# Optimization experiments

Hardware: AMD Instinct MI355X
Metric: run time of the kernel (lower is better)

Reference implementation:

```python
import jax, jax.numpy as jnp
import numpy as np

N_LAYERS = 6
D_MODEL = 272          # num_variables
D_STATE = 64           # d_state
D_INNER = 2 * D_MODEL  # expand=2 -> 544
D_CONV = 4
DT_RANK = 17           # ceil(272/16)
N_SCORES = 4
B, L = 4, 2048


def setup_inputs():
    key = jax.random.key(0)
    ks = jax.random.split(key, 10)
    def rn(k, shape, s=0.02):
        return jax.random.normal(k, shape, dtype=jnp.float32) * s
    A_init = jnp.broadcast_to(jnp.arange(1, D_STATE + 1, dtype=jnp.float32), (N_LAYERS, D_INNER, D_STATE))
    return {
        "x": jax.random.normal(ks[0], (B, L, D_MODEL), dtype=jnp.float32),
        "ln_w": jnp.ones((N_LAYERS, D_MODEL), jnp.float32),
        "ln_b": jnp.zeros((N_LAYERS, D_MODEL), jnp.float32),
        "in_proj_w": rn(ks[1], (N_LAYERS, 2 * D_INNER, D_MODEL)),
        "conv_w": rn(ks[2], (N_LAYERS, D_INNER, D_CONV), 0.2),
        "conv_b": jnp.zeros((N_LAYERS, D_INNER), jnp.float32),
        "x_proj_w": rn(ks[3], (N_LAYERS, DT_RANK + 2 * D_STATE, D_INNER)),
        "dt_proj_w": rn(ks[4], (N_LAYERS, D_INNER, DT_RANK), 0.1),
        "dt_proj_b": rn(ks[5], (N_LAYERS, D_INNER), 0.5),
        "A_log": jnp.log(A_init),
        "Dskip": jnp.ones((N_LAYERS, D_INNER), jnp.float32),
        "out_proj_w": rn(ks[6], (N_LAYERS, D_MODEL, D_INNER)),
        "reg_w": rn(ks[7], (N_SCORES, D_MODEL)),
        "reg_b": jnp.zeros((N_SCORES,), jnp.float32),
    }


def _layernorm(x, w, b, eps=1e-5):
    mu = x.mean(-1, keepdims=True)
    var = ((x - mu) ** 2).mean(-1, keepdims=True)
    return (x - mu) * jax.lax.rsqrt(var + eps) * w + b


def _selective_scan(u, delta, A, Bm, C, Dd):
    # u, delta: (b,l,d); Bm, C: (b,l,n); A: (d,n); Dd: (d,)
    def step(h, inp):
        d_t, B_t, C_t, u_t = inp                           # (b,d),(b,n),(b,n),(b,d)
        dA = jnp.exp(d_t[:, :, None] * A)                  # (b,d,n)
        h = dA * h + (d_t * u_t)[:, :, None] * B_t[:, None, :]
        return h, jnp.einsum('bdn,bn->bd', h, C_t)
    h0 = jnp.zeros((u.shape[0], A.shape[0], A.shape[1]), u.dtype)
    xs = tuple(jnp.swapaxes(a, 0, 1) for a in (delta, Bm, C, u))  # time-major
    _, ys = jax.lax.scan(step, h0, xs)
    return jnp.swapaxes(ys, 0, 1) + u * Dd


def _mamba_block(x, ln_w, ln_b, Wi, cw, cb, Wx, Wdt, bdt, A_log, Dd, Wo):
    h = _layernorm(x, ln_w, ln_b)
    xi, z = jnp.split(h @ Wi.T, 2, axis=-1)                # (b,l,d_inner) each
    xp = jnp.pad(xi, ((0, 0), (D_CONV - 1, 0), (0, 0)))    # causal depthwise conv
    xc = sum(xp[:, k:k + xi.shape[1], :] * cw[:, k] for k in range(D_CONV)) + cb
    xc = jax.nn.silu(xc)
    dbl = xc @ Wx.T                                        # (b,l,dt_rank+2n)
    dt, Bm, C = jnp.split(dbl, [DT_RANK, DT_RANK + D_STATE], axis=-1)
    delta = jax.nn.softplus(dt @ Wdt.T + bdt)
    y = _selective_scan(xc, delta, -jnp.exp(A_log), Bm, C, Dd)
    y = y * jax.nn.silu(z)
    return x + y @ Wo.T                                    # residual


def reference(x, ln_w, ln_b, in_proj_w, conv_w, conv_b, x_proj_w, dt_proj_w, dt_proj_b, A_log, Dskip, out_proj_w, reg_w, reg_b):
    for i in range(N_LAYERS):
        x = _mamba_block(x, ln_w[i], ln_b[i], in_proj_w[i], conv_w[i], conv_b[i],
                         x_proj_w[i], dt_proj_w[i], dt_proj_b[i], A_log[i], Dskip[i], out_proj_w[i])
    feat = x.mean(axis=1)                                  # (b, d_model)
    scores = feat @ reg_w.T + reg_b                        # (b, n_scores)
    return (scores, feat)
```

## Files before the change

kernel.cpp:

```cpp
#include <hip/hip_runtime.h>
#include <hip/hip_bf16.h>
#include <math.h>

#define NL 6
#define DM 272
#define DS 64
#define DI 544
#define DTR 17
#define NSC 4
#define BB 4
#define LL 2048
#define MTOK (BB*LL)
#define TCH 128
#define CH  16
#define DQ  (DI/4)

typedef __attribute__((ext_vector_type(8))) short bf16x8;
typedef __attribute__((ext_vector_type(4))) float f32x4;

__device__ __forceinline__ float sigmoidf_(float x){ return 1.0f/(1.0f+__expf(-x)); }
__device__ __forceinline__ unsigned short f2bfu(float x){
    union { __hip_bfloat16 h; unsigned short u; } c; c.h = __float2bfloat16(x); return c.u;
}
__device__ __forceinline__ float bfu2f(unsigned short u){ return __uint_as_float(((unsigned)u)<<16); }
__device__ __forceinline__ float exp2x(float x){ float r; asm("v_exp_f32 %0, %1" : "=v"(r) : "v"(x)); return r; }
__device__ __forceinline__ float log2x(float x){ float r; asm("v_log_f32 %0, %1" : "=v"(r) : "v"(x)); return r; }
__device__ __forceinline__ float softplus_(float s){
    float sp = 0.6931471806f * log2x(1.0f + exp2x(s * 1.44269504f));
    return (s > 20.f) ? s : sp;
}

#define DPPADD(x, ctrl) x += __int_as_float(__builtin_amdgcn_update_dpp(0, __float_as_int(x), ctrl, 0xf, 0xf, true))
__device__ __forceinline__ float wsum64(float x){
    DPPADD(x, 0x111); DPPADD(x, 0x112); DPPADD(x, 0x114); DPPADD(x, 0x118);
    DPPADD(x, 0x142); DPPADD(x, 0x143);
    return x;
}

__global__ __launch_bounds__(256) void ln_kernel(const float* __restrict__ X,
                          const float* __restrict__ w,
                          const float* __restrict__ b,
                          unsigned short* __restrict__ Hb)
{
    int wave = threadIdx.x >> 6;
    int lane = threadIdx.x & 63;
    int tok = blockIdx.x*4 + wave;
    const float* xr = X + (size_t)tok*DM;
    float v[5];
    float s=0.f, ss=0.f;
    #pragma unroll
    for (int j=0;j<5;++j){
        int idx = lane + j*64;
        float x = (idx < DM) ? xr[idx] : 0.f;
        v[j]=x; s+=x; ss+=x*x;
    }
    #pragma unroll
    for (int off=1; off<64; off<<=1){ s += __shfl_xor(s,off); ss += __shfl_xor(ss,off); }
    float mu  = s * (1.0f/DM);
    float var = ss*(1.0f/DM) - mu*mu;
    float inv = 1.0f/sqrtf(var + 1e-5f);
    unsigned short* hr = Hb + (size_t)tok*DM;
    #pragma unroll
    for (int j=0;j<5;++j){
        int idx = lane + j*64;
        if (idx<DM) hr[idx] = f2bfu((v[j]-mu)*inv*w[idx] + b[idx]);
    }
}

template<bool RESID, bool OUTBF16>
__global__ __launch_bounds__(256) void gmfma(const unsigned short* __restrict__ A, int lda,
                     const unsigned short* __restrict__ W, int ldw,
                     void* __restrict__ Cv, int ldc,
                     const float* __restrict__ R, int ldr,
                     int N, int K)
{
    __shared__ unsigned short As[128*40];
    __shared__ unsigned short Bs[128*40];
    int bm = blockIdx.x*128, bn = blockIdx.y*128;
    int tid = threadIdx.x;
    int lane = tid & 63, wave = tid >> 6;
    int wm = wave >> 1, wn = wave & 1;
    f32x4 acc[4][4] = {};
    int r16 = lane & 15, kg = (lane >> 4) * 8;
    for (int k0=0; k0<K; k0+=32){
        #pragma unroll
        for (int it=0; it<2; ++it){
            int cid = tid + it*256;
            int row = cid >> 2, kq = (cid & 3)*8;
            int kk = k0 + kq;
            uint4 za = make_uint4(0,0,0,0);
            if (kk < K) za = *(const uint4*)(A + (size_t)(bm+row)*lda + kk);
            *(uint4*)&As[row*40 + kq] = za;
            uint4 zb = make_uint4(0,0,0,0);
            int wr = bn + row;
            if (wr < N && kk < K) zb = *(const uint4*)(W + (size_t)wr*ldw + kk);
            *(uint4*)&Bs[row*40 + kq] = zb;
        }
        __syncthreads();
        bf16x8 af[4], bfr[4];
        #pragma unroll
        for (int mi=0; mi<4; ++mi)
            af[mi] = *(bf16x8*)&As[(wm*64 + mi*16 + r16)*40 + kg];
        #pragma unroll
        for (int ni=0; ni<4; ++ni)
            bfr[ni] = *(bf16x8*)&Bs[(wn*64 + ni*16 + r16)*40 + kg];
        #pragma unroll
        for (int mi=0; mi<4; ++mi)
            #pragma unroll
            for (int ni=0; ni<4; ++ni)
                acc[mi][ni] = __builtin_amdgcn_mfma_f32_16x16x32_bf16(af[mi], bfr[ni], acc[mi][ni], 0, 0, 0);
        __syncthreads();
    }
    int rowt = (lane >> 4)*4, colt = lane & 15;
    #pragma unroll
    for (int mi=0; mi<4; ++mi){
        #pragma unroll
        for (int ni=0; ni<4; ++ni){
            int col = bn + wn*64 + ni*16 + colt;
            if (col < N){
                #pragma unroll
                for (int j=0; j<4; ++j){
                    int row = bm + wm*64 + mi*16 + rowt + j;
                    float v = acc[mi][ni][j];
                    if (RESID) v += R[(size_t)row*ldr + col];
                    if (OUTBF16)
                        ((unsigned short*)Cv)[(size_t)row*ldc + col] = f2bfu(v);
                    else
                        ((float*)Cv)[(size_t)row*ldc + col] = v;
                }
            }
        }
    }
}

__global__ __launch_bounds__(256) void conv_t2_kernel(const unsigned short* __restrict__ XZb,
                                 const float* __restrict__ cw,
                                 const float* __restrict__ cb,
                                 unsigned int* __restrict__ UGt,
                                 unsigned short* __restrict__ XCb)
{
    __shared__ float xi[67][69];
    __shared__ float zz[64][69];
    int bid = blockIdx.x;
    int b  = bid >> 8;
    int rem = bid & 255;
    int t0 = (rem >> 3)*64;
    int d0 = (rem & 7)*68;
    int tid = threadIdx.x;
    for (int li = tid; li < 67*17; li += 256){
        int row = li / 17, q = li - row*17;
        int tg = t0 - 3 + row;
        float4 v = make_float4(0.f,0.f,0.f,0.f);
        if (tg >= 0){
            ushort4 u4 = *(const ushort4*)(XZb + ((size_t)b*LL + tg)*(2*DI) + d0 + q*4);
            v.x = bfu2f(u4.x); v.y = bfu2f(u4.y); v.z = bfu2f(u4.z); v.w = bfu2f(u4.w);
        }
        xi[row][q*4+0]=v.x; xi[row][q*4+1]=v.y; xi[row][q*4+2]=v.z; xi[row][q*4+3]=v.w;
    }
    for (int li = tid; li < 64*17; li += 256){
        int row = li / 17, q = li - row*17;
        ushort4 u4 = *(const ushort4*)(XZb + ((size_t)b*LL + t0 + row)*(2*DI) + DI + d0 + q*4);
        zz[row][q*4+0]=bfu2f(u4.x); zz[row][q*4+1]=bfu2f(u4.y);
        zz[row][q*4+2]=bfu2f(u4.z); zz[row][q*4+3]=bfu2f(u4.w);
    }
    __syncthreads();
    int t = tid & 63;
    int dw = tid >> 6;
    float xcreg[17];
    #pragma unroll
    for (int i=0; i<17; ++i){
        int dl = dw + i*4;
        int d = d0 + dl;
        const float* cwd = cw + d*4;
        float acc = cb[d];
        #pragma unroll
        for (int k=0;k<4;++k) acc = fmaf(xi[t+k][dl], cwd[k], acc);
        float xc = acc * sigmoidf_(acc);
        float z  = zz[t][dl];
        size_t o = ((size_t)b*DI + d)*LL + t0 + t;
        float g = z * sigmoidf_(z);
        UGt[o] = (unsigned int)f2bfu(xc) | ((unsigned int)f2bfu(g) << 16);
        xcreg[i] = xc;
    }
    __syncthreads();
    #pragma unroll
    for (int i=0; i<17; ++i) zz[t][dw + i*4] = xcreg[i];
    __syncthreads();
    for (int li = tid; li < 64*17; li += 256){
        int row = li / 17, q = li - row*17;
        ushort4 v;
        v.x = f2bfu(zz[row][q*4+0]); v.y = f2bfu(zz[row][q*4+1]);
        v.z = f2bfu(zz[row][q*4+2]); v.w = f2bfu(zz[row][q*4+3]);
        *(ushort4*)&XCb[((size_t)b*LL + t0 + row)*DI + d0 + q*4] = v;
    }
}

__global__ __launch_bounds__(256) void scan_a(const unsigned int* __restrict__ UGt,
                       const float* __restrict__ DBLb,
                       const float* __restrict__ Wdt,
                       const float* __restrict__ bdt,
                       const float* __restrict__ A_log,
                       float* __restrict__ Q,
                       float* __restrict__ S,
                       unsigned short* __restrict__ DELtb)
{
    __shared__ float2 dlb[4][4][64];
    int tid = threadIdx.x;
    int wave = tid >> 6, lane = tid & 63;
    float2 (*Db)[64] = dlb[wave];
    int wid = blockIdx.x*4 + wave;
    int dd = wid % DQ;
    int c  = (wid / DQ) % CH;
    int b  = wid / (DQ*CH);
    int d0 = dd, d1 = dd+DQ, d2 = dd+2*DQ, d3 = dd+3*DQ;
    const float L2E = 1.44269504f;
    float Av0 = -__expf(A_log[d0*DS + lane]) * L2E;
    float Av1 = -__expf(A_log[d1*DS + lane]) * L2E;
    float Av2 = -__expf(A_log[d2*DS + lane]) * L2E;
    float Av3 = -__expf(A_log[d3*DS + lane]) * L2E;
    const float* wd0 = Wdt + d0*DTR;
    const float* wd1 = Wdt + d1*DTR;
    const float* wd2 = Wdt + d2*DTR;
    const float* wd3 = Wdt + d3*DTR;
    float h0=0.f,h1=0.f,h2=0.f,h3=0.f, ds0=0.f,ds1=0.f,ds2=0.f,ds3=0.f;
    size_t rb0 = ((size_t)b*DI + d0)*LL + c*TCH;
    size_t rb1 = ((size_t)b*DI + d1)*LL + c*TCH;
    size_t rb2 = ((size_t)b*DI + d2)*LL + c*TCH;
    size_t rb3 = ((size_t)b*DI + d3)*LL + c*TCH;
    const float* pB = DBLb + ((size_t)b*LL + (size_t)c*TCH)*145;
    for (int blk=0; blk<TCH/64; ++blk){
        const float* dp = pB + (size_t)(blk*64 + lane)*145;
        float s0=bdt[d0], s1=bdt[d1], s2=bdt[d2], s3=bdt[d3];
        #pragma unroll
        for (int r=0;r<17;++r){
            float d = dp[r];
            s0 = fmaf(d, wd0[r], s0);
            s1 = fmaf(d, wd1[r], s1);
            s2 = fmaf(d, wd2[r], s2);
            s3 = fmaf(d, wd3[r], s3);
        }
        float dl0 = softplus_(s0), dl1 = softplus_(s1);
        float dl2 = softplus_(s2), dl3 = softplus_(s3);
        size_t o0 = rb0 + blk*64 + lane, o1 = rb1 + blk*64 + lane;
        size_t o2 = rb2 + blk*64 + lane, o3 = rb3 + blk*64 + lane;
        DELtb[o0] = f2bfu(dl0); DELtb[o1] = f2bfu(dl1);
        DELtb[o2] = f2bfu(dl2); DELtb[o3] = f2bfu(dl3);
        float du0 = dl0*bfu2f((unsigned short)UGt[o0]);
        float du1 = dl1*bfu2f((unsigned short)UGt[o1]);
        float du2 = dl2*bfu2f((unsigned short)UGt[o2]);
        float du3 = dl3*bfu2f((unsigned short)UGt[o3]);
        ds0 += dl0; ds1 += dl1; ds2 += dl2; ds3 += dl3;
        Db[0][lane] = make_float2(dl0, du0);
        Db[1][lane] = make_float2(dl1, du1);
        Db[2][lane] = make_float2(dl2, du2);
        Db[3][lane] = make_float2(dl3, du3);
        const float* p = pB + (size_t)blk*64*145;
        #pragma unroll 1
        for (int g=0; g<8; ++g){
            const float2* q0 = &Db[0][g*8];
            const float2* q1 = &Db[1][g*8];
            const float2* q2 = &Db[2][g*8];
            const float2* q3 = &Db[3][g*8];
            #pragma unroll
            for (int i=0; i<8; ++i){
                float Bv = p[17+lane];
                float2 a0=q0[i], a1=q1[i], a2=q2[i], a3=q3[i];
                h0 = fmaf(exp2x(a0.x*Av0), h0, a0.y*Bv);
                h1 = fmaf(exp2x(a1.x*Av1), h1, a1.y*Bv);
                h2 = fmaf(exp2x(a2.x*Av2), h2, a2.y*Bv);
                h3 = fmaf(exp2x(a3.x*Av3), h3, a3.y*Bv);
                p += 145;
            }
        }
    }
    size_t q0i = ((size_t)b*DI + d0)*CH + c, q1i = ((size_t)b*DI + d1)*CH + c;
    size_t q2i = ((size_t)b*DI + d2)*CH + c, q3i = ((size_t)b*DI + d3)*CH + c;
    Q[q0i*64 + lane] = h0; Q[q1i*64 + lane] = h1;
    Q[q2i*64 + lane] = h2; Q[q3i*64 + lane] = h3;
    float s0w = wsum64(ds0), s1w = wsum64(ds1), s2w = wsum64(ds2), s3w = wsum64(ds3);
    if (lane == 63){ S[q0i]=s0w; S[q1i]=s1w; S[q2i]=s2w; S[q3i]=s3w; }
}

__global__ __launch_bounds__(256) void scan_c(const unsigned int* __restrict__ UGt,
                       const unsigned short* __restrict__ DELtb,
                       const float* __restrict__ DBLb,
                       const float* __restrict__ A_log,
                       const float* __restrict__ Dskip,
                       const float* __restrict__ Q,
                       const float* __restrict__ S,
                       unsigned short* __restrict__ Yb)
{
    __shared__ float P[4][2][4][76];
    __shared__ float Ypark[4][2][4];
    __shared__ float2 dlb[4][2][64];
    __shared__ unsigned short Yst[64][12];
    int tid = threadIdx.x;
    int wave = tid >> 6, lane = tid & 63;
    float (*Pr0)[76] = P[wave][0];
    float (*Pr1)[76] = P[wave][1];
    float* Yp0 = Ypark[wave][0];
    float* Yp1 = Ypark[wave][1];
    float2* Db0 = dlb[wave][0];
    float2* Db1 = dlb[wave][1];
    int wid = blockIdx.x*4 + wave;
    int dd = wid % (DI/2);
    int c  = (wid / (DI/2)) % CH;
    int b  = wid / ((DI/2)*CH);
    int d0 = dd, d1 = dd + DI/2;
    int wid0 = blockIdx.x*4;
    int dd0b = wid0 % (DI/2);
    int cB = (wid0 / (DI/2)) % CH;
    int bB = wid0 / ((DI/2)*CH);
    const float L2E = 1.44269504f;
    float Av0 = -__expf(A_log[d0*DS + lane]) * L2E;
    float Av1 = -__expf(A_log[d1*DS + lane]) * L2E;
    float Dd0 = Dskip[d0], Dd1 = Dskip[d1];
    size_t q0 = ((size_t)b*DI + d0)*CH, q1 = ((size_t)b*DI + d1)*CH;
    float h0=0.f, h1=0.f;
    for (int j=0; j<c; ++j){
        h0 = fmaf(exp2x(Av0*S[q0+j]), h0, Q[(q0+j)*64 + lane]);
        h1 = fmaf(exp2x(Av1*S[q1+j]), h1, Q[(q1+j)*64 + lane]);
    }
    size_t rb0 = ((size_t)b*DI + d0)*LL + c*TCH;
    size_t rb1 = ((size_t)b*DI + d1)*LL + c*TCH;
    const float* pB = DBLb + ((size_t)b*LL + c*TCH)*145;
    int fr = lane >> 4, fq = (lane & 15)*4;
    for (int blk=0; blk<TCH/64; ++blk){
        size_t o0 = rb0 + blk*64 + lane, o1 = rb1 + blk*64 + lane;
        float dl0 = bfu2f(DELtb[o0]), dl1 = bfu2f(DELtb[o1]);
        unsigned int ug0 = UGt[o0], ug1 = UGt[o1];
        float ul0 = bfu2f((unsigned short)ug0), ul1 = bfu2f((unsigned short)ug1);
        float gl0 = bfu2f((unsigned short)(ug0 >> 16)), gl1 = bfu2f((unsigned short)(ug1 >> 16));
        Db0[lane] = make_float2(dl0, dl0*ul0);
        Db1[lane] = make_float2(dl1, dl1*ul1);
        float y0=0.f, y1=0.f;
        const float* p = pB + (size_t)blk*64*145;
        #pragma unroll 1
        for (int f=0; f<16; ++f){
            const float2* db0 = &Db0[f*4];
            const float2* db1 = &Db1[f*4];
            #pragma unroll
            for (int i=0; i<4; ++i){
                float Bv = p[17+lane];
                float Cv = p[81+lane];
                float2 a0 = db0[i], a1 = db1[i];
                h0 = fmaf(exp2x(a0.x*Av0), h0, a0.y*Bv);
                h1 = fmaf(exp2x(a1.x*Av1), h1, a1.y*Bv);
                Pr0[i][lane] = h0*Cv;
                Pr1[i][lane] = h1*Cv;
                p += 145;
            }
            float4 xa0 = *(const float4*)&Pr0[fr][fq];
            float s0f = (xa0.x+xa0.y)+(xa0.z+xa0.w);
            DPPADD(s0f,0x111); DPPADD(s0f,0x112); DPPADD(s0f,0x114); DPPADD(s0f,0x118);
            float4 xa1 = *(const float4*)&Pr1[fr][fq];
            float s1f = (xa1.x+xa1.y)+(xa1.z+xa1.w);
            DPPADD(s1f,0x111); DPPADD(s1f,0x112); DPPADD(s1f,0x114); DPPADD(s1f,0x118);
            if ((lane & 15) == 15){ Yp0[fr] = s0f; Yp1[fr] = s1f; }
            float g0 = Yp0[lane & 3];
            float g1 = Yp1[lane & 3];
            if ((lane >> 2) == f){ y0 = g0; y1 = g1; }
        }
        Yst[lane][wave]     = f2bfu((y0 + ul0*Dd0)*gl0);
        Yst[lane][4 + wave] = f2bfu((y1 + ul1*Dd1)*gl1);
        __syncthreads();
        if (tid < 128){
            int row = tid & 63, grp = tid >> 6;
            ushort4 v = *(const ushort4*)&Yst[row][grp*4];
            size_t trow = (size_t)bB*LL + (size_t)cB*TCH + blk*64 + row;
            *(ushort4*)&Yb[trow*DI + dd0b + grp*(DI/2)] = v;
        }
        __syncthreads();
    }
}

__global__ __launch_bounds__(256) void wconv_kernel(const float* __restrict__ src,
                            unsigned short* __restrict__ dst,
                            int total, int kin, int kout)
{
    int idx = blockIdx.x*256 + threadIdx.x;
    if (idx >= total) return;
    int r = idx / kout, c = idx - r*kout;
    float v = (c < kin) ? src[(size_t)r*kin + c] : 0.f;
    dst[idx] = f2bfu(v);
}

__global__ __launch_bounds__(256) void head1_kernel(const float* __restrict__ X,
                             float* __restrict__ Pt)
{
    int b = blockIdx.x >> 6, c = blockIdx.x & 63;
    int tid = threadIdx.x;
    for (int dm = tid; dm < DM; dm += 256){
        float s = 0.f;
        const float* base = X + ((size_t)b*LL + c*32)*DM + dm;
        #pragma unroll 8
        for (int tt=0; tt<32; ++tt) s += base[(size_t)tt*DM];
        Pt[(size_t)(b*64 + c)*DM + dm] = s;
    }
}

__global__ __launch_bounds__(256) void head2_kernel(const float* __restrict__ Pt,
                             const float* __restrict__ reg_w,
                             const float* __restrict__ reg_b,
                             float* __restrict__ out)
{
    __shared__ float feat[DM];
    int b = blockIdx.x, tid = threadIdx.x;
    for (int dm = tid; dm < DM; dm += 256){
        float s = 0.f;
        for (int c=0; c<64; ++c) s += Pt[(size_t)(b*64 + c)*DM + dm];
        float f = s * (1.0f/LL);
        feat[dm] = f;
        out[16 + b*DM + dm] = f;
    }
    __syncthreads();
    if (tid < NSC){
        float s = reg_b[tid];
        const float* wr = reg_w + tid*DM;
        for (int k=0;k<DM;++k) s = fmaf(feat[k], wr[k], s);
        out[b*NSC + tid] = s;
    }
}

extern "C" void kernel_launch(void* const* d_in, const int* in_sizes, int n_in,
                              void* d_out, int out_size, void* d_ws, size_t ws_size,
                              hipStream_t stream)
{
    const float* x_in  = (const float*)d_in[0];
    const float* ln_w  = (const float*)d_in[1];
    const float* ln_b  = (const float*)d_in[2];
    const float* Wi    = (const float*)d_in[3];
    const float* cw    = (const float*)d_in[4];
    const float* cb    = (const float*)d_in[5];
    const float* Wx    = (const float*)d_in[6];
    const float* Wdt   = (const float*)d_in[7];
    const float* bdt   = (const float*)d_in[8];
    const float* A_log = (const float*)d_in[9];
    const float* Dd    = (const float*)d_in[10];
    const float* Wo    = (const float*)d_in[11];
    const float* regw  = (const float*)d_in[12];
    const float* regb  = (const float*)d_in[13];
    float* out = (float*)d_out;

    char* base = (char*)d_ws;
    auto carve = [&](size_t bytes) -> char* {
        char* p = base; base += (bytes + 255) & ~(size_t)255; return p;
    };
    unsigned short* XZb   = (unsigned short*)carve((size_t)MTOK*1088*2);
    unsigned int*   UGt   = (unsigned int*)carve((size_t)MTOK*544*4);
    unsigned short* DELtb = (unsigned short*)carve((size_t)MTOK*544*2);
    float*          DBLb  = (float*)carve((size_t)MTOK*145*4);
    float*          Xb    = (float*)carve((size_t)MTOK*272*4);
    unsigned short* Yb    = (unsigned short*)carve((size_t)MTOK*544*2);
    char*           SCR   = carve((size_t)MTOK*272*4);
    float*          Sbuf  = (float*)carve((size_t)BB*DI*CH*4);
    unsigned short* WiB   = (unsigned short*)carve((size_t)NL*1088*DM*2);
    unsigned short* WxB   = (unsigned short*)carve((size_t)NL*145*DI*2);
    unsigned short* WoB   = (unsigned short*)carve((size_t)NL*272*DI*2);

    unsigned short* Hb  = (unsigned short*)SCR;
    unsigned short* XCb = (unsigned short*)SCR;
    float*          Q   = (float*)SCR;
    float*          Pt  = (float*)SCR;

    (void)hipMemcpyAsync(Xb, x_in, sizeof(float)*(size_t)MTOK*DM, hipMemcpyDeviceToDevice, stream);

    wconv_kernel<<<(NL*1088*DM + 255)/256, 256, 0, stream>>>(Wi, WiB, NL*1088*DM, DM, DM);
    wconv_kernel<<<(NL*145*DI + 255)/256, 256, 0, stream>>>(Wx, WxB, NL*145*DI, DI, DI);
    wconv_kernel<<<(NL*272*DI + 255)/256, 256, 0, stream>>>(Wo, WoB, NL*272*DI, DI, DI);

    for (int l=0; l<NL; ++l){
        ln_kernel<<<MTOK/4, 256, 0, stream>>>(Xb, ln_w + l*DM, ln_b + l*DM, Hb);
        gmfma<false,true><<<dim3(MTOK/128, (2*DI+127)/128), 256, 0, stream>>>(
            Hb, DM, WiB + (size_t)l*2*DI*DM, DM, XZb, 2*DI, nullptr, 0, 2*DI, DM);
        conv_t2_kernel<<<BB*256, 256, 0, stream>>>(XZb, cw + l*DI*4, cb + l*DI, UGt, XCb);
        gmfma<false,false><<<dim3(MTOK/128, 2), 256, 0, stream>>>(
            XCb, DI, WxB + (size_t)l*145*DI, DI, DBLb, 145, nullptr, 0, 145, DI);
        scan_a<<<(BB*CH*DQ)/4, 256, 0, stream>>>(UGt, DBLb, Wdt + (size_t)l*DI*DTR, bdt + l*DI,
                                                 A_log + (size_t)l*DI*DS, Q, Sbuf, DELtb);
        scan_c<<<(BB*CH*(DI/2))/4, 256, 0, stream>>>(UGt, DELtb, DBLb,
                                                     A_log + (size_t)l*DI*DS, Dd + l*DI, Q, Sbuf, Yb);
        gmfma<true,false><<<dim3(MTOK/128, 3), 256, 0, stream>>>(
            Yb, DI, WoB + (size_t)l*DM*DI, DI, Xb, DM, Xb, DM, DM, DI);
    }
    head1_kernel<<<BB*64, 256, 0, stream>>>(Xb, Pt);
    head2_kernel<<<BB, 256, 0, stream>>>(Pt, regw, regb, out);
}
```

Baseline: 1.460 ms.

## Split x_proj output into dt buffer and packed bf16 B/C pairs for scans

The x_proj GEMM epilogue now writes the dt part to a compact fp32 buffer of 17 columns and packs B and C as interleaved bf16 pairs into one 32-bit word per state. The scan kernels read one packed word per lane per timestep instead of two separate fp32 loads at a 145-float stride, which cuts scan memory traffic and load count. scan_c also reads the delta/u pairs from shared memory as float4. The trade-off is lower precision for B and C, plus scattered 2-byte stores in the GEMM epilogue.

```diff
diff --git a/kernel.cpp b/kernel.cpp
--- a/kernel.cpp
+++ b/kernel.cpp
@@ -23,6 +23,8 @@
     union { __hip_bfloat16 h; unsigned short u; } c; c.h = __float2bfloat16(x); return c.u;
 }
 __device__ __forceinline__ float bfu2f(unsigned short u){ return __uint_as_float(((unsigned)u)<<16); }
+__device__ __forceinline__ float bclo(unsigned int bc){ return __uint_as_float(bc << 16); }
+__device__ __forceinline__ float bchi(unsigned int bc){ return __uint_as_float(bc & 0xffff0000u); }
 __device__ __forceinline__ float exp2x(float x){ float r; asm("v_exp_f32 %0, %1" : "=v"(r) : "v"(x)); return r; }
 __device__ __forceinline__ float log2x(float x){ float r; asm("v_log_f32 %0, %1" : "=v"(r) : "v"(x)); return r; }
 __device__ __forceinline__ float softplus_(float s){
@@ -67,11 +69,12 @@
     }
 }
 
-template<bool RESID, bool OUTBF16>
+template<int OMODE, bool RESID>
 __global__ __launch_bounds__(256) void gmfma(const unsigned short* __restrict__ A, int lda,
                      const unsigned short* __restrict__ W, int ldw,
                      void* __restrict__ Cv, int ldc,
                      const float* __restrict__ R, int ldr,
+                     void* __restrict__ aux,
                      int N, int K)
 {
     __shared__ unsigned short As[128*40];
@@ -123,10 +126,18 @@
                     int row = bm + wm*64 + mi*16 + rowt + j;
                     float v = acc[mi][ni][j];
                     if (RESID) v += R[(size_t)row*ldr + col];
-                    if (OUTBF16)
+                    if (OMODE == 0)
+                        ((float*)Cv)[(size_t)row*ldc + col] = v;
+                    else if (OMODE == 1)
                         ((unsigned short*)Cv)[(size_t)row*ldc + col] = f2bfu(v);
-                    else
-                        ((float*)Cv)[(size_t)row*ldc + col] = v;
+                    else {
+                        if (col < DTR)
+                            ((float*)Cv)[(size_t)row*DTR + col] = v;
+                        else if (col < DTR + DS)
+                            ((unsigned short*)aux)[((size_t)row*DS + col - DTR)*2] = f2bfu(v);
+                        else
+                            ((unsigned short*)aux)[((size_t)row*DS + col - DTR - DS)*2 + 1] = f2bfu(v);
+                    }
                 }
             }
         }
@@ -196,7 +207,8 @@
 }
 
 __global__ __launch_bounds__(256) void scan_a(const unsigned int* __restrict__ UGt,
-                       const float* __restrict__ DBLb,
+                       const float* __restrict__ DTb,
+                       const unsigned int* __restrict__ BCb,
                        const float* __restrict__ Wdt,
                        const float* __restrict__ bdt,
                        const float* __restrict__ A_log,
@@ -204,7 +216,7 @@
                        float* __restrict__ S,
                        unsigned short* __restrict__ DELtb)
 {
-    __shared__ float2 dlb[4][4][64];
+    __shared__ __align__(16) float2 dlb[4][4][64];
     int tid = threadIdx.x;
     int wave = tid >> 6, lane = tid & 63;
     float2 (*Db)[64] = dlb[wave];
@@ -223,13 +235,13 @@
     const float* wd2 = Wdt + d2*DTR;
     const float* wd3 = Wdt + d3*DTR;
     float h0=0.f,h1=0.f,h2=0.f,h3=0.f, ds0=0.f,ds1=0.f,ds2=0.f,ds3=0.f;
+    size_t tokBase = (size_t)b*LL + (size_t)c*TCH;
     size_t rb0 = ((size_t)b*DI + d0)*LL + c*TCH;
     size_t rb1 = ((size_t)b*DI + d1)*LL + c*TCH;
     size_t rb2 = ((size_t)b*DI + d2)*LL + c*TCH;
     size_t rb3 = ((size_t)b*DI + d3)*LL + c*TCH;
-    const float* pB = DBLb + ((size_t)b*LL + (size_t)c*TCH)*145;
     for (int blk=0; blk<TCH/64; ++blk){
-        const float* dp = pB + (size_t)(blk*64 + lane)*145;
+        const float* dp = DTb + (tokBase + blk*64 + lane)*DTR;
         float s0=bdt[d0], s1=bdt[d1], s2=bdt[d2], s3=bdt[d3];
         #pragma unroll
         for (int r=0;r<17;++r){
@@ -254,7 +266,7 @@
         Db[1][lane] = make_float2(dl1, du1);
         Db[2][lane] = make_float2(dl2, du2);
         Db[3][lane] = make_float2(dl3, du3);
-        const float* p = pB + (size_t)blk*64*145;
+        const unsigned int* pbc = BCb + (tokBase + blk*64)*DS;
         #pragma unroll 1
         for (int g=0; g<8; ++g){
             const float2* q0 = &Db[0][g*8];
@@ -263,13 +275,13 @@
             const float2* q3 = &Db[3][g*8];
             #pragma unroll
             for (int i=0; i<8; ++i){
-                float Bv = p[17+lane];
+                float Bv = bclo(pbc[lane]);
                 float2 a0=q0[i], a1=q1[i], a2=q2[i], a3=q3[i];
                 h0 = fmaf(exp2x(a0.x*Av0), h0, a0.y*Bv);
                 h1 = fmaf(exp2x(a1.x*Av1), h1, a1.y*Bv);
                 h2 = fmaf(exp2x(a2.x*Av2), h2, a2.y*Bv);
                 h3 = fmaf(exp2x(a3.x*Av3), h3, a3.y*Bv);
-                p += 145;
+                pbc += DS;
             }
         }
     }
@@ -283,7 +295,7 @@
 
 __global__ __launch_bounds__(256) void scan_c(const unsigned int* __restrict__ UGt,
                        const unsigned short* __restrict__ DELtb,
-                       const float* __restrict__ DBLb,
+                       const unsigned int* __restrict__ BCb,
                        const float* __restrict__ A_log,
                        const float* __restrict__ Dskip,
                        const float* __restrict__ Q,
@@ -292,7 +304,7 @@
 {
     __shared__ float P[4][2][4][76];
     __shared__ float Ypark[4][2][4];
-    __shared__ float2 dlb[4][2][64];
+    __shared__ __align__(16) float2 dlb[4][2][64];
     __shared__ unsigned short Yst[64][12];
     int tid = threadIdx.x;
     int wave = tid >> 6, lane = tid & 63;
@@ -321,9 +333,9 @@
         h0 = fmaf(exp2x(Av0*S[q0+j]), h0, Q[(q0+j)*64 + lane]);
         h1 = fmaf(exp2x(Av1*S[q1+j]), h1, Q[(q1+j)*64 + lane]);
     }
+    size_t tokBase = (size_t)b*LL + (size_t)c*TCH;
     size_t rb0 = ((size_t)b*DI + d0)*LL + c*TCH;
     size_t rb1 = ((size_t)b*DI + d1)*LL + c*TCH;
-    const float* pB = DBLb + ((size_t)b*LL + c*TCH)*145;
     int fr = lane >> 4, fq = (lane & 15)*4;
     for (int blk=0; blk<TCH/64; ++blk){
         size_t o0 = rb0 + blk*64 + lane, o1 = rb1 + blk*64 + lane;
@@ -334,21 +346,27 @@
         Db0[lane] = make_float2(dl0, dl0*ul0);
         Db1[lane] = make_float2(dl1, dl1*ul1);
         float y0=0.f, y1=0.f;
-        const float* p = pB + (size_t)blk*64*145;
+        const unsigned int* pbc = BCb + (tokBase + blk*64)*DS;
         #pragma unroll 1
         for (int f=0; f<16; ++f){
-            const float2* db0 = &Db0[f*4];
-            const float2* db1 = &Db1[f*4];
+            float4 pa0 = *(const float4*)&Db0[f*4];
+            float4 pa1 = *(const float4*)&Db0[f*4+2];
+            float4 pb0 = *(const float4*)&Db1[f*4];
+            float4 pb1 = *(const float4*)&Db1[f*4+2];
             #pragma unroll
             for (int i=0; i<4; ++i){
-                float Bv = p[17+lane];
-                float Cv = p[81+lane];
-                float2 a0 = db0[i], a1 = db1[i];
-                h0 = fmaf(exp2x(a0.x*Av0), h0, a0.y*Bv);
-                h1 = fmaf(exp2x(a1.x*Av1), h1, a1.y*Bv);
+                unsigned int bc = pbc[lane];
+                float Bv = bclo(bc);
+                float Cv = bchi(bc);
+                float d0v = (i==0)?pa0.x:(i==1)?pa0.z:(i==2)?pa1.x:pa1.z;
+                float u0v = (i==0)?pa0.y:(i==1)?pa0.w:(i==2)?pa1.y:pa1.w;
+                float d1v = (i==0)?pb0.x:(i==1)?pb0.z:(i==2)?pb1.x:pb1.z;
+                float u1v = (i==0)?pb0.y:(i==1)?pb0.w:(i==2)?pb1.y:pb1.w;
+                h0 = fmaf(exp2x(d0v*Av0), h0, u0v*Bv);
+                h1 = fmaf(exp2x(d1v*Av1), h1, u1v*Bv);
                 Pr0[i][lane] = h0*Cv;
                 Pr1[i][lane] = h1*Cv;
-                p += 145;
+                pbc += DS;
             }
             float4 xa0 = *(const float4*)&Pr0[fr][fq];
             float s0f = (xa0.x+xa0.y)+(xa0.z+xa0.w);
@@ -449,7 +467,8 @@
     unsigned short* XZb   = (unsigned short*)carve((size_t)MTOK*1088*2);
     unsigned int*   UGt   = (unsigned int*)carve((size_t)MTOK*544*4);
     unsigned short* DELtb = (unsigned short*)carve((size_t)MTOK*544*2);
-    float*          DBLb  = (float*)carve((size_t)MTOK*145*4);
+    float*          DTb   = (float*)carve((size_t)MTOK*DTR*4);
+    unsigned int*   BCb   = (unsigned int*)carve((size_t)MTOK*DS*4);
     float*          Xb    = (float*)carve((size_t)MTOK*272*4);
     unsigned short* Yb    = (unsigned short*)carve((size_t)MTOK*544*2);
     char*           SCR   = carve((size_t)MTOK*272*4);
@@ -471,17 +490,17 @@
 
     for (int l=0; l<NL; ++l){
         ln_kernel<<<MTOK/4, 256, 0, stream>>>(Xb, ln_w + l*DM, ln_b + l*DM, Hb);
-        gmfma<false,true><<<dim3(MTOK/128, (2*DI+127)/128), 256, 0, stream>>>(
-            Hb, DM, WiB + (size_t)l*2*DI*DM, DM, XZb, 2*DI, nullptr, 0, 2*DI, DM);
+        gmfma<1,false><<<dim3(MTOK/128, (2*DI+127)/128), 256, 0, stream>>>(
+            Hb, DM, WiB + (size_t)l*2*DI*DM, DM, XZb, 2*DI, nullptr, 0, nullptr, 2*DI, DM);
         conv_t2_kernel<<<BB*256, 256, 0, stream>>>(XZb, cw + l*DI*4, cb + l*DI, UGt, XCb);
-        gmfma<false,false><<<dim3(MTOK/128, 2), 256, 0, stream>>>(
-            XCb, DI, WxB + (size_t)l*145*DI, DI, DBLb, 145, nullptr, 0, 145, DI);
-        scan_a<<<(BB*CH*DQ)/4, 256, 0, stream>>>(UGt, DBLb, Wdt + (size_t)l*DI*DTR, bdt + l*DI,
+        gmfma<2,false><<<dim3(MTOK/128, 2), 256, 0, stream>>>(
+            XCb, DI, WxB + (size_t)l*145*DI, DI, DTb, DTR, nullptr, 0, BCb, 145, DI);
+        scan_a<<<(BB*CH*DQ)/4, 256, 0, stream>>>(UGt, DTb, BCb, Wdt + (size_t)l*DI*DTR, bdt + l*DI,
                                                  A_log + (size_t)l*DI*DS, Q, Sbuf, DELtb);
-        scan_c<<<(BB*CH*(DI/2))/4, 256, 0, stream>>>(UGt, DELtb, DBLb,
+        scan_c<<<(BB*CH*(DI/2))/4, 256, 0, stream>>>(UGt, DELtb, BCb,
                                                      A_log + (size_t)l*DI*DS, Dd + l*DI, Q, Sbuf, Yb);
-        gmfma<true,false><<<dim3(MTOK/128, 3), 256, 0, stream>>>(
-            Yb, DI, WoB + (size_t)l*DM*DI, DI, Xb, DM, Xb, DM, DM, DI);
+        gmfma<0,true><<<dim3(MTOK/128, 3), 256, 0, stream>>>(
+            Yb, DI, WoB + (size_t)l*DM*DI, DI, Xb, DM, Xb, DM, nullptr, DM, DI);
     }
     head1_kernel<<<BB*64, 256, 0, stream>>>(Xb, Pt);
     head2_kernel<<<BB, 256, 0, stream>>>(Pt, regw, regb, out);
```

After: 1.407 ms, median of 2. 3.6% less time.
